# Optimization experiments

Measured on AMD Instinct MI355X. Metric: run time of the kernel, lower is better.

## Reference

```python
import jax, jax.numpy as jnp
import numpy as np

N, L, H, Q = 64, 258, 1024, 256
WINDOW = 16.0
DEV_POW = 128.0  # 2 * (window/2)^2, Luong local-p sigma = D/2


def setup_inputs() -> dict:
    key = jax.random.key(0)
    k1, k2, k3, k4, k5, k6 = jax.random.split(key, 6)
    encoder_outputs = jax.random.normal(k1, (N, L, H), dtype=jnp.float32)
    decoder_h_t = jax.random.normal(k2, (N, Q, H), dtype=jnp.float32)
    src_len = jax.random.randint(k3, (N,), 32, L + 1).astype(jnp.int32)
    # window centers within each source sentence
    p_t = jax.random.uniform(k4, (N,), dtype=jnp.float32) * (src_len.astype(jnp.float32) - 1.0)
    W_a = jax.random.normal(k5, (H, H), dtype=jnp.float32) * (1.0 / np.sqrt(H))
    W_c = jax.random.normal(k6, (H, 2 * H), dtype=jnp.float32) * (1.0 / np.sqrt(2 * H))
    return {"encoder_outputs": encoder_outputs, "decoder_h_t": decoder_h_t,
            "src_len": src_len, "p_t": p_t, "W_a": W_a, "W_c": W_c}


def reference(encoder_outputs, decoder_h_t, src_len, p_t, W_a, W_c):
    n, l, h = encoder_outputs.shape
    idx = jnp.arange(l, dtype=jnp.float32)  # index_matrix, length == max_length == L

    # local_p window: [p_t - D, p_t + D], clamped to [0, src_len]
    src_end = src_len.astype(jnp.float32)
    attn_start = jnp.maximum(p_t - WINDOW, 0.0)          # [N]
    attn_end = jnp.minimum(p_t + WINDOW, src_end)        # [N]
    mask = (idx[None, :] < attn_start[:, None]) | (idx[None, :] > attn_end[:, None])  # [N,L]

    # Luong 'general' score: h_t^T W_a h_s -> [N,Q,L]
    score = jnp.einsum('nqh,hk,nlk->nql', decoder_h_t, W_a, encoder_outputs)

    score = jnp.where(mask[:, None, :], -1e9, score)
    align = jax.nn.softmax(score, axis=2)                 # [N,Q,L]

    # gaussian reweighting centered at p_t
    gauss = jnp.exp(-((idx[None, :] - p_t[:, None]) ** 2) / DEV_POW)  # [N,L]
    align = align * gauss[:, None, :]

    context = jnp.einsum('nql,nlh->nqh', align, encoder_outputs)      # [N,Q,H]
    cat = jnp.concatenate([context, decoder_h_t], axis=2)             # [N,Q,2H]
    return jnp.tanh(cat @ W_c.T)                                      # [N,Q,H]
```

## Files before the change

kernel.cpp:

```cpp
#include <hip/hip_runtime.h>
#include <hip/hip_bf16.h>
#include <cstdint>

#define DEVINL __device__ __forceinline__

typedef __attribute__((ext_vector_type(8))) short short8;
typedef __attribute__((ext_vector_type(4))) float f32x4;
typedef __attribute__((ext_vector_type(4))) unsigned short u16x4;

static constexpr int NB = 64, LL = 258, HH = 1024, QQ = 256;
static constexpr int WROWS = 33;
static constexpr int MU = 2176;
static constexpr int VTN = 4096;

static constexpr size_t OFF_META = 0;
static constexpr size_t SZ_WE   = (size_t)MU * HH * 2;
static constexpr size_t OFF_WEHI = 1024;
static constexpr size_t OFF_WELO = OFF_WEHI + SZ_WE;
static constexpr size_t OFF_WAHI = OFF_WELO + SZ_WE;
static constexpr size_t OFF_WALO = OFF_WAHI + (size_t)HH * HH * 2;
static constexpr size_t OFF_WCBF = OFF_WALO + (size_t)HH * HH * 2;
static constexpr size_t OFF_HBF  = OFF_WCBF + (size_t)HH * 2 * HH * 2;
static constexpr size_t OFF_U    = OFF_HBF + (size_t)NB * QQ * HH * 2;
static constexpr size_t OFF_UHI  = OFF_U;
static constexpr size_t OFF_ULO  = OFF_U + (size_t)MU * HH * 2;
static constexpr size_t OFF_PHL  = OFF_U + (size_t)MU * HH * 4;
static constexpr size_t OFF_VT   = OFF_PHL + (size_t)NB * QQ * 128 * 2;

DEVINL unsigned short f2bf(float x) {
    union { float f; uint32_t u; } v; v.f = x;
    uint32_t u = v.u;
    uint32_t r = (u + 0x7FFFu + ((u >> 16) & 1u)) >> 16;
    return (unsigned short)r;
}
DEVINL float bf2f(unsigned short b) {
    union { uint32_t u; float f; } v; v.u = ((uint32_t)b) << 16;
    return v.f;
}

template <typename T>
DEVINL void lds_load16(const T* g, T* l) {
    __builtin_amdgcn_global_load_lds(
        (const __attribute__((address_space(1))) void*)g,
        (__attribute__((address_space(3))) void*)l, 16, 0, 0);
}

DEVINL float fast_tanh(float x) {
    float e = __expf(2.0f * x);
    return 1.0f - 2.0f / (e + 1.0f);
}

DEVINL void window_of(float p, int sl, int& ls, int& lc) {
    float se = (float)sl;
    float s = fmaxf(p - 16.0f, 0.0f);
    float e = fminf(p + 16.0f, se);
    ls = (int)ceilf(s);
    int le = (int)floorf(e); if (le > LL - 1) le = LL - 1;
    lc = le - ls + 1;
    if (lc < 0) lc = 0;
    if (lc > WROWS) lc = WROWS;
}

__global__ __launch_bounds__(256) void k_prep(const float* __restrict__ enc,
                                              const float* __restrict__ pt,
                                              const int* __restrict__ slen,
                                              const float* __restrict__ Wa,
                                              const float* __restrict__ Wc,
                                              unsigned short* __restrict__ wehi,
                                              unsigned short* __restrict__ welo,
                                              unsigned short* __restrict__ wahi,
                                              unsigned short* __restrict__ walo,
                                              unsigned short* __restrict__ wcbf) {
    const int b = blockIdx.x, t = threadIdx.x;
    if (b < MU) {
        int r = b;
        const float* src = nullptr;
        bool valid = false;
        if (r < NB * WROWS) {
            int n = r / WROWS, li = r - n * WROWS;
            int ls, lc;
            window_of(pt[n], slen[n], ls, lc);
            if (li < lc) { valid = true; src = enc + ((size_t)n * LL + ls + li) * HH; }
        }
        f32x4 v;
        if (valid) v = ((const f32x4*)src)[t];
        else { v[0] = 0.f; v[1] = 0.f; v[2] = 0.f; v[3] = 0.f; }
        u16x4 h, l;
#pragma unroll
        for (int j = 0; j < 4; ++j) {
            unsigned short hb = f2bf(v[j]);
            h[j] = hb;
            l[j] = f2bf(v[j] - bf2f(hb));
        }
        size_t o = (size_t)r * HH / 4 + t;
        ((u16x4*)wehi)[o] = h;
        ((u16x4*)welo)[o] = l;
    } else if (b < MU + 1024) {
        int i = (b - MU) * 256 + t;
        f32x4 v = ((const f32x4*)Wa)[i];
        u16x4 h, l;
#pragma unroll
        for (int j = 0; j < 4; ++j) {
            unsigned short hb = f2bf(v[j]);
            h[j] = hb;
            l[j] = f2bf(v[j] - bf2f(hb));
        }
        ((u16x4*)wahi)[i] = h;
        ((u16x4*)walo)[i] = l;
    } else {
        int i = (b - MU - 1024) * 256 + t;
        f32x4 v = ((const f32x4*)Wc)[i];
        u16x4 h;
#pragma unroll
        for (int j = 0; j < 4; ++j) h[j] = f2bf(v[j]);
        ((u16x4*)wcbf)[i] = h;
    }
}

__global__ __launch_bounds__(256) void k_wgemm(const unsigned short* __restrict__ wehi,
                                               const unsigned short* __restrict__ welo,
                                               const unsigned short* __restrict__ wahi,
                                               const unsigned short* __restrict__ walo,
                                               const unsigned short* __restrict__ wcbf,
                                               unsigned short* __restrict__ Uhi,
                                               unsigned short* __restrict__ Ulo,
                                               unsigned short* __restrict__ VT) {
    __shared__ unsigned short smem[24576];
    const int tid = threadIdx.x;
    const int bid = blockIdx.x;

    const int w = tid >> 6, lane = tid & 63;
    const int wr = w >> 1, wc = w & 1;
    const int r16 = lane & 15, khalf = lane >> 4, rg = lane >> 4;
    const int srow = tid >> 2;
    const int scol = ((tid & 3) ^ ((tid >> 3) & 3)) * 8;
    const int kslot = (khalf ^ ((r16 >> 1) & 3)) * 8;

    if (bid < 272) {
        const int m0 = (bid >> 3) * 64;
        const int n0 = (bid & 7) * 128;
        f32x4 acc[2][4] = {};

        auto stage = [&](int buf, int kb) {
            lds_load16(wehi + (size_t)(m0 + srow) * HH + kb + scol, &smem[buf * 2048 + tid * 8]);
            lds_load16(welo + (size_t)(m0 + srow) * HH + kb + scol, &smem[4096 + buf * 2048 + tid * 8]);
#pragma unroll
            for (int i = 0; i < 2; ++i) {
                lds_load16(wahi + (size_t)(n0 + i * 64 + srow) * HH + kb + scol,
                           &smem[8192 + buf * 4096 + i * 2048 + tid * 8]);
                lds_load16(walo + (size_t)(n0 + i * 64 + srow) * HH + kb + scol,
                           &smem[16384 + buf * 4096 + i * 2048 + tid * 8]);
            }
        };

        stage(0, 0);
        for (int t = 0; t < 32; ++t) {
            const int buf = t & 1;
            asm volatile("s_waitcnt vmcnt(0)" ::: "memory");
            __builtin_amdgcn_s_barrier();
            short8 ah[2], al[2], bh[4], bl[4];
#pragma unroll
            for (int f = 0; f < 2; ++f) {
                int ai = buf * 2048 + (wr * 32 + f * 16 + r16) * 32 + kslot;
                ah[f] = *(const short8*)&smem[ai];
                al[f] = *(const short8*)&smem[4096 + ai];
            }
#pragma unroll
            for (int nf = 0; nf < 4; ++nf) {
                int bi = buf * 4096 + (wc * 64 + nf * 16 + r16) * 32 + kslot;
                bh[nf] = *(const short8*)&smem[8192 + bi];
                bl[nf] = *(const short8*)&smem[16384 + bi];
            }
            if (t + 1 < 32) stage(buf ^ 1, (t + 1) * 32);
            asm volatile("s_waitcnt lgkmcnt(0)" ::: "memory");
            __builtin_amdgcn_sched_barrier(0);
#pragma unroll
            for (int mf = 0; mf < 2; ++mf)
#pragma unroll
                for (int nf = 0; nf < 4; ++nf) {
                    acc[mf][nf] = __builtin_amdgcn_mfma_f32_16x16x32_bf16(ah[mf], bh[nf], acc[mf][nf], 0, 0, 0);
                    acc[mf][nf] = __builtin_amdgcn_mfma_f32_16x16x32_bf16(ah[mf], bl[nf], acc[mf][nf], 0, 0, 0);
                    acc[mf][nf] = __builtin_amdgcn_mfma_f32_16x16x32_bf16(al[mf], bh[nf], acc[mf][nf], 0, 0, 0);
                }
            __builtin_amdgcn_s_barrier();
        }
#pragma unroll
        for (int mf = 0; mf < 2; ++mf)
#pragma unroll
            for (int nf = 0; nf < 4; ++nf)
#pragma unroll
                for (int r = 0; r < 4; ++r) {
                    int m = m0 + wr * 32 + mf * 16 + rg * 4 + r;
                    int nn = n0 + wc * 64 + nf * 16 + r16;
                    float v = acc[mf][nf][r];
                    unsigned short h = f2bf(v);
                    Uhi[(size_t)m * HH + nn] = h;
                    Ulo[(size_t)m * HH + nn] = f2bf(v - bf2f(h));
                }
    } else {
        const int b2 = bid - 272;
        const int m0 = (b2 / 17) * 64;
        const int n0 = (b2 % 17) * 128;
        f32x4 acc[2][4] = {};

        auto stage = [&](int buf, int kb) {
            lds_load16(wcbf + (size_t)(m0 + srow) * (2 * HH) + kb + scol, &smem[buf * 2048 + tid * 8]);
#pragma unroll
            for (int i = 0; i < 2; ++i) {
                lds_load16(wehi + (size_t)(n0 + i * 64 + srow) * HH + kb + scol,
                           &smem[8192 + buf * 4096 + i * 2048 + tid * 8]);
                lds_load16(welo + (size_t)(n0 + i * 64 + srow) * HH + kb + scol,
                           &smem[16384 + buf * 4096 + i * 2048 + tid * 8]);
            }
        };

        stage(0, 0);
        for (int t = 0; t < 32; ++t) {
            const int buf = t & 1;
            asm volatile("s_waitcnt vmcnt(0)" ::: "memory");
            __builtin_amdgcn_s_barrier();
            short8 af[2], bh[4], bl[4];
#pragma unroll
            for (int f = 0; f < 2; ++f)
                af[f] = *(const short8*)&smem[buf * 2048 + (wr * 32 + f * 16 + r16) * 32 + kslot];
#pragma unroll
            for (int nf = 0; nf < 4; ++nf) {
                int bi = buf * 4096 + (wc * 64 + nf * 16 + r16) * 32 + kslot;
                bh[nf] = *(const short8*)&smem[8192 + bi];
                bl[nf] = *(const short8*)&smem[16384 + bi];
            }
            if (t + 1 < 32) stage(buf ^ 1, (t + 1) * 32);
            asm volatile("s_waitcnt lgkmcnt(0)" ::: "memory");
            __builtin_amdgcn_sched_barrier(0);
#pragma unroll
            for (int mf = 0; mf < 2; ++mf)
#pragma unroll
                for (int nf = 0; nf < 4; ++nf) {
                    acc[mf][nf] = __builtin_amdgcn_mfma_f32_16x16x32_bf16(af[mf], bh[nf], acc[mf][nf], 0, 0, 0);
                    acc[mf][nf] = __builtin_amdgcn_mfma_f32_16x16x32_bf16(af[mf], bl[nf], acc[mf][nf], 0, 0, 0);
                }
            __builtin_amdgcn_s_barrier();
        }
#pragma unroll
        for (int mf = 0; mf < 2; ++mf)
#pragma unroll
            for (int nf = 0; nf < 4; ++nf)
#pragma unroll
                for (int r = 0; r < 4; ++r) {
                    int o = m0 + wr * 32 + mf * 16 + rg * 4 + r;
                    int wrow = n0 + wc * 64 + nf * 16 + r16;
                    int n = wrow / WROWS, li = wrow - n * WROWS;
                    if (n < NB)
                        VT[(size_t)o * VTN + n * 64 + li] = f2bf(acc[mf][nf][r]);
                }
    }
}

__global__ __launch_bounds__(256) void k_attn2(const float* __restrict__ ht,
                                               const unsigned short* __restrict__ Uhi,
                                               const unsigned short* __restrict__ Ulo,
                                               const float* __restrict__ pt,
                                               const int* __restrict__ slen,
                                               unsigned short* __restrict__ Phl,
                                               unsigned short* __restrict__ hbf) {
    __shared__ float sPart[4][32 * 48];
    __shared__ float sScore[32 * 48];

    const int tid = threadIdx.x;
    const int w = tid >> 6, lane = tid & 63;
    const int n = blockIdx.x >> 3, q0 = (blockIdx.x & 7) * 32;
    int ls, lc;
    window_of(pt[n], slen[n], ls, lc);
    const float p = pt[n];
    const int r16 = lane & 15, khalf = lane >> 4, rg = lane >> 4;

    const float* hbase = ht + ((size_t)(n * QQ + q0)) * HH;
    unsigned short* hbbase = hbf + ((size_t)(n * QQ + q0)) * HH;
    const unsigned short* uhbase = Uhi + (size_t)n * WROWS * HH;
    const unsigned short* ulbase = Ulo + (size_t)n * WROWS * HH;

    f32x4 acc[2][3] = {};
    for (int ks = 0; ks < 8; ++ks) {
        int kcol = w * 256 + ks * 32 + khalf * 8;
        short8 ah[2], al[2];
#pragma unroll
        for (int mf = 0; mf < 2; ++mf) {
            const float* src = hbase + (size_t)(mf * 16 + r16) * HH + kcol;
            f32x4 v0 = *(const f32x4*)src;
            f32x4 v1 = *(const f32x4*)(src + 4);
            float vv[8] = {v0[0], v0[1], v0[2], v0[3], v1[0], v1[1], v1[2], v1[3]};
#pragma unroll
            for (int j = 0; j < 8; ++j) {
                unsigned short hb = f2bf(vv[j]);
                ah[mf][j] = (short)hb;
                al[mf][j] = (short)f2bf(vv[j] - bf2f(hb));
            }
            *(short8*)(hbbase + (size_t)(mf * 16 + r16) * HH + kcol) = ah[mf];
        }
#pragma unroll
        for (int nf = 0; nf < 3; ++nf) {
            size_t uoff = (size_t)(nf * 16 + r16) * HH + kcol;
            short8 bh = *(const short8*)(uhbase + uoff);
            short8 bl = *(const short8*)(ulbase + uoff);
#pragma unroll
            for (int mf = 0; mf < 2; ++mf) {
                acc[mf][nf] = __builtin_amdgcn_mfma_f32_16x16x32_bf16(ah[mf], bh, acc[mf][nf], 0, 0, 0);
                acc[mf][nf] = __builtin_amdgcn_mfma_f32_16x16x32_bf16(ah[mf], bl, acc[mf][nf], 0, 0, 0);
                acc[mf][nf] = __builtin_amdgcn_mfma_f32_16x16x32_bf16(al[mf], bh, acc[mf][nf], 0, 0, 0);
            }
        }
    }
#pragma unroll
    for (int mf = 0; mf < 2; ++mf)
#pragma unroll
        for (int nf = 0; nf < 3; ++nf)
#pragma unroll
            for (int r = 0; r < 4; ++r)
                sPart[w][(mf * 16 + rg * 4 + r) * 48 + nf * 16 + r16] = acc[mf][nf][r];
    __syncthreads();

    {
        int q = tid >> 3, g = tid & 7;
        float sc6[6];
#pragma unroll
        for (int s = 0; s < 6; ++s) {
            int li = g + 8 * s;
            int o = q * 48 + li;
            sc6[s] = sPart[0][o] + sPart[1][o] + sPart[2][o] + sPart[3][o];
        }
        float mx = -1e30f;
#pragma unroll
        for (int s = 0; s < 6; ++s) { int li = g + 8 * s; if (li < lc) mx = fmaxf(mx, sc6[s]); }
        for (int off = 1; off < 8; off <<= 1) mx = fmaxf(mx, __shfl_xor(mx, off, 8));
        float sum = 0.f, ex[6];
#pragma unroll
        for (int s = 0; s < 6; ++s) {
            int li = g + 8 * s;
            float e = (li < lc) ? __expf(sc6[s] - mx) : 0.f;
            ex[s] = e; sum += e;
        }
        for (int off = 1; off < 8; off <<= 1) sum += __shfl_xor(sum, off, 8);
        float inv = 1.0f / sum;
#pragma unroll
        for (int s = 0; s < 6; ++s) {
            int li = g + 8 * s;
            float d = (float)(ls + li) - p;
            float gs = __expf(-(d * d) * (1.0f / 128.0f));
            sScore[q * 48 + li] = ex[s] * inv * gs;
        }
    }
    __syncthreads();

    {
        int row = tid >> 3, c0 = (tid & 7) * 8;
        short8 ph, pl;
#pragma unroll
        for (int j = 0; j < 8; ++j) {
            int c = c0 + j;
            float pv = (c < 48) ? sScore[row * 48 + c] : 0.f;
            unsigned short hb = f2bf(pv);
            ph[j] = (short)hb;
            pl[j] = (short)f2bf(pv - bf2f(hb));
        }
        size_t base = (size_t)(n * QQ + q0 + row) * 128;
        *(short8*)&Phl[base + c0] = ph;
        *(short8*)&Phl[base + 64 + c0] = pl;
    }
}

__global__ __launch_bounds__(256) void k_out_gemm128(
    const unsigned short* __restrict__ Ahf,
    const unsigned short* __restrict__ Bt,
    const unsigned short* __restrict__ Phl,
    const unsigned short* __restrict__ VT,
    float* __restrict__ out) {
    __shared__ unsigned short sA[128 * 64], sB[128 * 64];

    const int tid = threadIdx.x;
    const int wid = tid >> 6, lane = tid & 63;
    const int bid = blockIdx.x;
    const int swz = (bid & 7) * 128 + (bid >> 3);
    const int mt = swz >> 3, nt = swz & 7;
    const int m0 = mt * 128, n0 = nt * 128;
    const int nb = mt >> 1;
    const int wr = wid >> 1, wc = wid & 1;
    const int r16 = lane & 15, kg = lane >> 4;

    const int srow8 = lane >> 3;
    const int kswz = ((lane & 7) ^ srow8) * 8;

    f32x4 acc[4][4] = {};

    for (int t = 0; t < 18; ++t) {
        if (t > 0) __syncthreads();
        if (t < 16) {
            const int kb = t * 64;
#pragma unroll
            for (int i = 0; i < 4; ++i) {
                int row = i * 32 + wid * 8 + srow8;
                lds_load16(Ahf + (size_t)(m0 + row) * HH + kb + kswz,
                           &sA[i * 2048 + wid * 512]);
                lds_load16(Bt + (size_t)(n0 + row) * (2 * HH) + 1024 + kb + kswz,
                           &sB[i * 2048 + wid * 512]);
            }
        } else {
            const int pc = (t - 16) * 64;
#pragma unroll
            for (int i = 0; i < 4; ++i) {
                int row = i * 32 + wid * 8 + srow8;
                lds_load16(Phl + (size_t)(m0 + row) * 128 + pc + kswz,
                           &sA[i * 2048 + wid * 512]);
                lds_load16(VT + (size_t)(n0 + row) * VTN + nb * 64 + kswz,
                           &sB[i * 2048 + wid * 512]);
            }
        }
        asm volatile("s_waitcnt vmcnt(0)" ::: "memory");
        __syncthreads();

        short8 a[4][2];
#pragma unroll
        for (int mq = 0; mq < 4; ++mq)
#pragma unroll
            for (int ks = 0; ks < 2; ++ks)
                a[mq][ks] = *(const short8*)&sA[(wr * 64 + mq * 16 + r16) * 64 +
                                                (((ks * 4 + kg) ^ (r16 & 7)) * 8)];
#pragma unroll
        for (int nq = 0; nq < 4; ++nq) {
            short8 b0 = *(const short8*)&sB[(wc * 64 + nq * 16 + r16) * 64 +
                                            (((0 + kg) ^ (r16 & 7)) * 8)];
            short8 b1 = *(const short8*)&sB[(wc * 64 + nq * 16 + r16) * 64 +
                                            (((4 + kg) ^ (r16 & 7)) * 8)];
#pragma unroll
            for (int mq = 0; mq < 4; ++mq) {
                acc[mq][nq] = __builtin_amdgcn_mfma_f32_16x16x32_bf16(a[mq][0], b0, acc[mq][nq], 0, 0, 0);
                acc[mq][nq] = __builtin_amdgcn_mfma_f32_16x16x32_bf16(a[mq][1], b1, acc[mq][nq], 0, 0, 0);
            }
        }
    }

#pragma unroll
    for (int mq = 0; mq < 4; ++mq)
#pragma unroll
        for (int nq = 0; nq < 4; ++nq) {
            int row = m0 + wr * 64 + mq * 16 + kg * 4;
            int col = n0 + wc * 64 + nq * 16 + r16;
#pragma unroll
            for (int r = 0; r < 4; ++r)
                out[(size_t)(row + r) * HH + col] = fast_tanh(acc[mq][nq][r]);
        }
}

extern "C" void kernel_launch(void* const* d_in, const int* in_sizes, int n_in,
                              void* d_out, int out_size, void* d_ws, size_t ws_size,
                              hipStream_t stream) {
    const float* enc  = (const float*)d_in[0];
    const float* ht   = (const float*)d_in[1];
    const int*   slen = (const int*)d_in[2];
    const float* pt   = (const float*)d_in[3];
    const float* Wa   = (const float*)d_in[4];
    const float* Wc   = (const float*)d_in[5];
    float* out = (float*)d_out;

    char* ws = (char*)d_ws;
    unsigned short* wehi = (unsigned short*)(ws + OFF_WEHI);
    unsigned short* welo = (unsigned short*)(ws + OFF_WELO);
    unsigned short* wahi = (unsigned short*)(ws + OFF_WAHI);
    unsigned short* walo = (unsigned short*)(ws + OFF_WALO);
    unsigned short* wcbf = (unsigned short*)(ws + OFF_WCBF);
    unsigned short* hbf  = (unsigned short*)(ws + OFF_HBF);
    unsigned short* uhi  = (unsigned short*)(ws + OFF_UHI);
    unsigned short* ulo  = (unsigned short*)(ws + OFF_ULO);
    unsigned short* phl  = (unsigned short*)(ws + OFF_PHL);
    unsigned short* vt   = (unsigned short*)(ws + OFF_VT);

    hipLaunchKernelGGL(k_prep, dim3(MU + 1024 + 2048), dim3(256), 0, stream,
                       enc, pt, slen, Wa, Wc, wehi, welo, wahi, walo, wcbf);
    hipLaunchKernelGGL(k_wgemm, dim3(544), dim3(256), 0, stream,
                       wehi, welo, wahi, walo, wcbf, uhi, ulo, vt);
    hipLaunchKernelGGL(k_attn2, dim3(NB * 8), dim3(256), 0, stream,
                       ht, uhi, ulo, pt, slen, phl, hbf);
    hipLaunchKernelGGL(k_out_gemm128, dim3(1024), dim3(256), 0, stream,
                       hbf, wcbf, phl, vt, out);
}
```

Measured before the change: 138.5 us.

## Split U-GEMM into its own 64x64 kernel and co-schedule VT GEMM with attention

```diff
diff --git a/kernel.cpp b/kernel.cpp
--- a/kernel.cpp
+++ b/kernel.cpp
@@ -117,90 +117,104 @@
     }
 }
 
-__global__ __launch_bounds__(256) void k_wgemm(const unsigned short* __restrict__ wehi,
-                                               const unsigned short* __restrict__ welo,
-                                               const unsigned short* __restrict__ wahi,
-                                               const unsigned short* __restrict__ walo,
-                                               const unsigned short* __restrict__ wcbf,
-                                               unsigned short* __restrict__ Uhi,
-                                               unsigned short* __restrict__ Ulo,
-                                               unsigned short* __restrict__ VT) {
-    __shared__ unsigned short smem[24576];
+__global__ __launch_bounds__(256) void k_ugemm64(const unsigned short* __restrict__ Ahi,
+                                                 const unsigned short* __restrict__ Alo,
+                                                 const unsigned short* __restrict__ Bhi,
+                                                 const unsigned short* __restrict__ Blo,
+                                                 unsigned short* __restrict__ Uhi,
+                                                 unsigned short* __restrict__ Ulo) {
+    __shared__ unsigned short sAh[2][64 * 32], sAl[2][64 * 32], sBh[2][64 * 32], sBl[2][64 * 32];
+    const int tid = threadIdx.x;
+    const int w = tid >> 6, lane = tid & 63;
+    const int m0 = blockIdx.y * 64, n0 = blockIdx.x * 64;
+    const int wr = w >> 1, wc = w & 1;
+    const int r16 = lane & 15, khalf = lane >> 4;
+    const int srow = tid >> 2;
+    const int scol = ((tid & 3) ^ ((tid >> 3) & 3)) * 8;
+    const int ldso = tid * 8;
+    const int kslot = (khalf ^ ((r16 >> 1) & 3)) * 8;
+    f32x4 acc[2][2] = {};
+
+    auto stage = [&](int buf, int kb) {
+        lds_load16(Ahi + (size_t)(m0 + srow) * HH + kb + scol, &sAh[buf][ldso]);
+        lds_load16(Alo + (size_t)(m0 + srow) * HH + kb + scol, &sAl[buf][ldso]);
+        lds_load16(Bhi + (size_t)(n0 + srow) * HH + kb + scol, &sBh[buf][ldso]);
+        lds_load16(Blo + (size_t)(n0 + srow) * HH + kb + scol, &sBl[buf][ldso]);
+    };
+
+    stage(0, 0);
+    for (int t = 0; t < 32; ++t) {
+        const int buf = t & 1;
+        asm volatile("s_waitcnt vmcnt(0)" ::: "memory");
+        __builtin_amdgcn_s_barrier();
+        short8 ah[2], al[2], bh[2], bl[2];
+#pragma unroll
+        for (int f = 0; f < 2; ++f) {
+            int ai = (wr * 32 + f * 16 + r16) * 32 + kslot;
+            ah[f] = *(const short8*)&sAh[buf][ai];
+            al[f] = *(const short8*)&sAl[buf][ai];
+            int bi = (wc * 32 + f * 16 + r16) * 32 + kslot;
+            bh[f] = *(const short8*)&sBh[buf][bi];
+            bl[f] = *(const short8*)&sBl[buf][bi];
+        }
+        if (t + 1 < 32) stage(buf ^ 1, (t + 1) * 32);
+        asm volatile("s_waitcnt lgkmcnt(0)" ::: "memory");
+        __builtin_amdgcn_sched_barrier(0);
+#pragma unroll
+        for (int mf = 0; mf < 2; ++mf)
+#pragma unroll
+            for (int nf = 0; nf < 2; ++nf) {
+                acc[mf][nf] = __builtin_amdgcn_mfma_f32_16x16x32_bf16(ah[mf], bh[nf], acc[mf][nf], 0, 0, 0);
+                acc[mf][nf] = __builtin_amdgcn_mfma_f32_16x16x32_bf16(ah[mf], bl[nf], acc[mf][nf], 0, 0, 0);
+                acc[mf][nf] = __builtin_amdgcn_mfma_f32_16x16x32_bf16(al[mf], bh[nf], acc[mf][nf], 0, 0, 0);
+            }
+        __builtin_amdgcn_s_barrier();
+    }
+    const int rg = lane >> 4;
+#pragma unroll
+    for (int mf = 0; mf < 2; ++mf)
+#pragma unroll
+        for (int nf = 0; nf < 2; ++nf)
+#pragma unroll
+            for (int r = 0; r < 4; ++r) {
+                int m = m0 + wr * 32 + mf * 16 + rg * 4 + r;
+                int nn = n0 + wc * 32 + nf * 16 + r16;
+                float v = acc[mf][nf][r];
+                unsigned short h = f2bf(v);
+                Uhi[(size_t)m * HH + nn] = h;
+                Ulo[(size_t)m * HH + nn] = f2bf(v - bf2f(h));
+            }
+}
+
+__global__ __launch_bounds__(256) void k_mix(const unsigned short* __restrict__ wehi,
+                                             const unsigned short* __restrict__ welo,
+                                             const unsigned short* __restrict__ wcbf,
+                                             const float* __restrict__ ht,
+                                             const unsigned short* __restrict__ Uhi,
+                                             const unsigned short* __restrict__ Ulo,
+                                             const float* __restrict__ pt,
+                                             const int* __restrict__ slen,
+                                             unsigned short* __restrict__ VT,
+                                             unsigned short* __restrict__ Phl,
+                                             unsigned short* __restrict__ hbf) {
+    __shared__ union {
+        unsigned short g[24576];
+        struct { float part[4][32 * 48]; float score[32 * 48]; } a;
+    } sm;
+
     const int tid = threadIdx.x;
     const int bid = blockIdx.x;
-
     const int w = tid >> 6, lane = tid & 63;
-    const int wr = w >> 1, wc = w & 1;
     const int r16 = lane & 15, khalf = lane >> 4, rg = lane >> 4;
-    const int srow = tid >> 2;
-    const int scol = ((tid & 3) ^ ((tid >> 3) & 3)) * 8;
-    const int kslot = (khalf ^ ((r16 >> 1) & 3)) * 8;
 
     if (bid < 272) {
-        const int m0 = (bid >> 3) * 64;
-        const int n0 = (bid & 7) * 128;
-        f32x4 acc[2][4] = {};
-
-        auto stage = [&](int buf, int kb) {
-            lds_load16(wehi + (size_t)(m0 + srow) * HH + kb + scol, &smem[buf * 2048 + tid * 8]);
-            lds_load16(welo + (size_t)(m0 + srow) * HH + kb + scol, &smem[4096 + buf * 2048 + tid * 8]);
-#pragma unroll
-            for (int i = 0; i < 2; ++i) {
-                lds_load16(wahi + (size_t)(n0 + i * 64 + srow) * HH + kb + scol,
-                           &smem[8192 + buf * 4096 + i * 2048 + tid * 8]);
-                lds_load16(walo + (size_t)(n0 + i * 64 + srow) * HH + kb + scol,
-                           &smem[16384 + buf * 4096 + i * 2048 + tid * 8]);
-            }
-        };
-
-        stage(0, 0);
-        for (int t = 0; t < 32; ++t) {
-            const int buf = t & 1;
-            asm volatile("s_waitcnt vmcnt(0)" ::: "memory");
-            __builtin_amdgcn_s_barrier();
-            short8 ah[2], al[2], bh[4], bl[4];
-#pragma unroll
-            for (int f = 0; f < 2; ++f) {
-                int ai = buf * 2048 + (wr * 32 + f * 16 + r16) * 32 + kslot;
-                ah[f] = *(const short8*)&smem[ai];
-                al[f] = *(const short8*)&smem[4096 + ai];
-            }
-#pragma unroll
-            for (int nf = 0; nf < 4; ++nf) {
-                int bi = buf * 4096 + (wc * 64 + nf * 16 + r16) * 32 + kslot;
-                bh[nf] = *(const short8*)&smem[8192 + bi];
-                bl[nf] = *(const short8*)&smem[16384 + bi];
-            }
-            if (t + 1 < 32) stage(buf ^ 1, (t + 1) * 32);
-            asm volatile("s_waitcnt lgkmcnt(0)" ::: "memory");
-            __builtin_amdgcn_sched_barrier(0);
-#pragma unroll
-            for (int mf = 0; mf < 2; ++mf)
-#pragma unroll
-                for (int nf = 0; nf < 4; ++nf) {
-                    acc[mf][nf] = __builtin_amdgcn_mfma_f32_16x16x32_bf16(ah[mf], bh[nf], acc[mf][nf], 0, 0, 0);
-                    acc[mf][nf] = __builtin_amdgcn_mfma_f32_16x16x32_bf16(ah[mf], bl[nf], acc[mf][nf], 0, 0, 0);
-                    acc[mf][nf] = __builtin_amdgcn_mfma_f32_16x16x32_bf16(al[mf], bh[nf], acc[mf][nf], 0, 0, 0);
-                }
-            __builtin_amdgcn_s_barrier();
-        }
-#pragma unroll
-        for (int mf = 0; mf < 2; ++mf)
-#pragma unroll
-            for (int nf = 0; nf < 4; ++nf)
-#pragma unroll
-                for (int r = 0; r < 4; ++r) {
-                    int m = m0 + wr * 32 + mf * 16 + rg * 4 + r;
-                    int nn = n0 + wc * 64 + nf * 16 + r16;
-                    float v = acc[mf][nf][r];
-                    unsigned short h = f2bf(v);
-                    Uhi[(size_t)m * HH + nn] = h;
-                    Ulo[(size_t)m * HH + nn] = f2bf(v - bf2f(h));
-                }
-    } else {
-        const int b2 = bid - 272;
-        const int m0 = (b2 / 17) * 64;
-        const int n0 = (b2 % 17) * 128;
+        unsigned short* smem = sm.g;
+        const int wr = w >> 1, wc = w & 1;
+        const int srow = tid >> 2;
+        const int scol = ((tid & 3) ^ ((tid >> 3) & 3)) * 8;
+        const int kslot = (khalf ^ ((r16 >> 1) & 3)) * 8;
+        const int m0 = (bid / 17) * 64;
+        const int n0 = (bid % 17) * 128;
         f32x4 acc[2][4] = {};
 
         auto stage = [&](int buf, int kb) {
@@ -247,32 +261,20 @@
             for (int nf = 0; nf < 4; ++nf)
 #pragma unroll
                 for (int r = 0; r < 4; ++r) {
-                    int o = m0 + wr * 32 + mf * 16 + rg * 4 + r;
-                    int wrow = n0 + wc * 64 + nf * 16 + r16;
+                    int o = m0 + (w >> 1) * 32 + mf * 16 + rg * 4 + r;
+                    int wrow = n0 + (w & 1) * 64 + nf * 16 + r16;
                     int n = wrow / WROWS, li = wrow - n * WROWS;
                     if (n < NB)
                         VT[(size_t)o * VTN + n * 64 + li] = f2bf(acc[mf][nf][r]);
                 }
-    }
-}
-
-__global__ __launch_bounds__(256) void k_attn2(const float* __restrict__ ht,
-                                               const unsigned short* __restrict__ Uhi,
-                                               const unsigned short* __restrict__ Ulo,
-                                               const float* __restrict__ pt,
-                                               const int* __restrict__ slen,
-                                               unsigned short* __restrict__ Phl,
-                                               unsigned short* __restrict__ hbf) {
-    __shared__ float sPart[4][32 * 48];
-    __shared__ float sScore[32 * 48];
-
-    const int tid = threadIdx.x;
-    const int w = tid >> 6, lane = tid & 63;
-    const int n = blockIdx.x >> 3, q0 = (blockIdx.x & 7) * 32;
+        return;
+    }
+
+    const int abid = bid - 272;
+    const int n = abid >> 3, q0 = (abid & 7) * 32;
     int ls, lc;
     window_of(pt[n], slen[n], ls, lc);
     const float p = pt[n];
-    const int r16 = lane & 15, khalf = lane >> 4, rg = lane >> 4;
 
     const float* hbase = ht + ((size_t)(n * QQ + q0)) * HH;
     unsigned short* hbbase = hbf + ((size_t)(n * QQ + q0)) * HH;
@@ -316,7 +318,7 @@
         for (int nf = 0; nf < 3; ++nf)
 #pragma unroll
             for (int r = 0; r < 4; ++r)
-                sPart[w][(mf * 16 + rg * 4 + r) * 48 + nf * 16 + r16] = acc[mf][nf][r];
+                sm.a.part[w][(mf * 16 + rg * 4 + r) * 48 + nf * 16 + r16] = acc[mf][nf][r];
     __syncthreads();
 
     {
@@ -326,7 +328,7 @@
         for (int s = 0; s < 6; ++s) {
             int li = g + 8 * s;
             int o = q * 48 + li;
-            sc6[s] = sPart[0][o] + sPart[1][o] + sPart[2][o] + sPart[3][o];
+            sc6[s] = sm.a.part[0][o] + sm.a.part[1][o] + sm.a.part[2][o] + sm.a.part[3][o];
         }
         float mx = -1e30f;
 #pragma unroll
@@ -346,7 +348,7 @@
             int li = g + 8 * s;
             float d = (float)(ls + li) - p;
             float gs = __expf(-(d * d) * (1.0f / 128.0f));
-            sScore[q * 48 + li] = ex[s] * inv * gs;
+            sm.a.score[q * 48 + li] = ex[s] * inv * gs;
         }
     }
     __syncthreads();
@@ -357,7 +359,7 @@
 #pragma unroll
         for (int j = 0; j < 8; ++j) {
             int c = c0 + j;
-            float pv = (c < 48) ? sScore[row * 48 + c] : 0.f;
+            float pv = (c < 48) ? sm.a.score[row * 48 + c] : 0.f;
             unsigned short hb = f2bf(pv);
             ph[j] = (short)hb;
             pl[j] = (short)f2bf(pv - bf2f(hb));
@@ -475,10 +477,10 @@
 
     hipLaunchKernelGGL(k_prep, dim3(MU + 1024 + 2048), dim3(256), 0, stream,
                        enc, pt, slen, Wa, Wc, wehi, welo, wahi, walo, wcbf);
-    hipLaunchKernelGGL(k_wgemm, dim3(544), dim3(256), 0, stream,
-                       wehi, welo, wahi, walo, wcbf, uhi, ulo, vt);
-    hipLaunchKernelGGL(k_attn2, dim3(NB * 8), dim3(256), 0, stream,
-                       ht, uhi, ulo, pt, slen, phl, hbf);
+    hipLaunchKernelGGL(k_ugemm64, dim3(HH / 64, MU / 64), dim3(256), 0, stream,
+                       wehi, welo, wahi, walo, uhi, ulo);
+    hipLaunchKernelGGL(k_mix, dim3(272 + NB * 8), dim3(256), 0, stream,
+                       wehi, welo, wcbf, ht, uhi, ulo, pt, slen, vt, phl, hbf);
     hipLaunchKernelGGL(k_out_gemm128, dim3(1024), dim3(256), 0, stream,
                        hbf, wcbf, phl, vt, out);
 }
```

Measured after the change: 146.8 us. 6.0% more time.
